# Optimization experiments

Measured on AMD Instinct MI355X. Metric: run time of the kernel, lower is better.

Reference implementation:

```python
import jax, jax.numpy as jnp
import numpy as np

N = 1000   # node count forced by fc1_1 in_features=1680 (see shape derivation)
E = 8000   # edges, avg degree ~8
F_IN = 6   # node feature dim (first 3 = pos, zeroed in forward)


def setup_inputs() -> dict:
    key = jax.random.key(0)
    ks = jax.random.split(key, 24)
    f = lambda k, s, sc=1.0: jax.random.normal(k, s, dtype=jnp.float32) * sc
    inp = {
        "x": f(ks[0], (N, F_IN)),
        "edge_index": jax.random.randint(ks[1], (2, E), 0, N, dtype=jnp.int64),
        # GCNConv weights (xavier-ish scale)
        "W1": f(ks[2], (F_IN, 32), 0.4), "b1": jnp.zeros((32,), jnp.float32),
        "W2": f(ks[3], (32, 32), 0.18), "b2": jnp.zeros((32,), jnp.float32),
        # Conv2d kernels, OIHW
        "k1": f(ks[4], (3, 1, 3, 2), 0.3), "kb1": jnp.zeros((3,), jnp.float32),
        "k2": f(ks[5], (6, 3, 3, 2), 0.2), "kb2": jnp.zeros((6,), jnp.float32),
        "k3": f(ks[6], (3, 6, 3, 2), 0.2), "kb3": jnp.zeros((3,), jnp.float32),
        "k4": f(ks[7], (1, 3, 3, 2), 0.2), "kb4": jnp.zeros((1,), jnp.float32),
        # FC head (torch Linear layout: [out, in])
        "fw1": f(ks[8], (1024, 1680), 0.02), "fb1": jnp.zeros((1024,), jnp.float32),
        "fw2": f(ks[9], (1024, 1024), 0.03), "fb2": jnp.zeros((1024,), jnp.float32),
        "fw3": f(ks[10], (64, 1024), 0.03), "fb3": jnp.zeros((64,), jnp.float32),
    }
    return inp


def _conv2d(x, w, b):
    out = jax.lax.conv_general_dilated(
        x, w, window_strides=(1, 1), padding="VALID",
        dimension_numbers=("NCHW", "OIHW", "NCHW"))
    return out + b[None, :, None, None]


def _maxpool2(x):  # MaxPool2d((2,1), stride=(2,1))
    return jax.lax.reduce_window(x, -jnp.inf, jax.lax.max,
                                 (1, 1, 2, 1), (1, 1, 2, 1), "VALID")


def reference(x, edge_index, W1, b1, W2, b2, k1, kb1, k2, kb2, k3, kb3, k4, kb4,
              fw1, fb1, fw2, fb2, fw3, fb3):
    num_nodes = x.shape[0]
    # forward zeroes the first 3 features (positions)
    x = x.at[:, :3].set(0.0)

    loop = jnp.arange(num_nodes)
    row = jnp.concatenate([edge_index[0], loop])
    col = jnp.concatenate([edge_index[1], loop])
    deg = jnp.zeros((num_nodes,), x.dtype).at[col].add(1.0)
    dinv = jnp.where(deg > 0, jax.lax.rsqrt(deg), 0.0)
    norm = (dinv[row] * dinv[col])[:, None]  # [E+N, 1]

    def gcn(h, W, b):
        hw = h @ W                                   # [N, 32]
        msg = hw[row] * norm                         # gather + scale
        return jax.ops.segment_sum(msg, col, num_segments=num_nodes) + b

    leaky = lambda v: jnp.where(v > 0, v, 0.2 * v)   # LeakyReLU(0.2)
    h = leaky(gcn(x, W1, b1))
    h = leaky(gcn(h, W2, b2))                        # [N, 32]

    img = h[None, None]                              # [1, 1, N, 32]
    img = _maxpool2(jax.nn.relu(_conv2d(img, k1, kb1)))   # [1,3,499,31]
    img = _maxpool2(jax.nn.relu(_conv2d(img, k2, kb2)))   # [1,6,248,30]
    img = _maxpool2(jax.nn.relu(_conv2d(img, k3, kb3)))   # [1,3,123,29]
    img = _maxpool2(jax.nn.relu(_conv2d(img, k4, kb4)))   # [1,1,60,28]

    v = img.reshape(-1)                              # [1680]
    v = v @ fw1.T + fb1                              # no activation between FCs (as in source)
    v = v @ fw2.T + fb2
    v = v @ fw3.T + fb3                              # [64]
    return v
```

## Files before the change

kernel.cpp:

```cpp
#include <hip/hip_runtime.h>

#define LEAKY(v) ((v) > 0.0f ? (v) : 0.2f * (v))

__global__ void k1_prep(const float* __restrict__ x, const int* __restrict__ col,
                        const float* __restrict__ W1, float* __restrict__ deg,
                        float* __restrict__ aggs ,
                        float* __restrict__ xw, int n, int E) {
    int tid = blockIdx.x * blockDim.x + threadIdx.x;
    int NT = gridDim.x * blockDim.x;
    for (int i = tid; i < 2 * n * 32; i += NT) aggs[i] = 0.0f;
    for (int e = tid; e < E; e += NT) atomicAdd(&deg[col[e]], 1.0f);
    for (int t = tid; t < n * 32; t += NT) {
        int j = t & 31, nn = t >> 5;
        xw[t] = x[nn*6+3] * W1[96+j]
              + x[nn*6+4] * W1[128+j]
              + x[nn*6+5] * W1[160+j];
    }
}

__global__ void k_scatter(const float* __restrict__ xw, const float* __restrict__ deg,
                          const int* __restrict__ row, const int* __restrict__ col,
                          float* __restrict__ agg, int E, int n) {
    int tid = blockIdx.x * blockDim.x + threadIdx.x;
    int total = (E + n) * 32;
    if (tid >= total) return;
    int e = tid >> 5, j = tid & 31;
    int r, c; float nrm;
    if (e < E) {
        r = row[e]; c = col[e];
        nrm = (1.0f / sqrtf(deg[r] + 1.0f)) * (1.0f / sqrtf(deg[c] + 1.0f));
    } else {
        r = c = e - E;
        nrm = 1.0f / (deg[r] + 1.0f);
    }
    atomicAdd(&agg[c * 32 + j], xw[r * 32 + j] * nrm);
}

__global__ void k3_xw2(const float* __restrict__ agg1, const float* __restrict__ b1,
                       const float* __restrict__ W2, float* __restrict__ xw, int n) {
    int tid = blockIdx.x * blockDim.x + threadIdx.x;
    if (tid >= n * 32) return;
    int j = tid & 31, nn = tid >> 5;
    const float* a = agg1 + nn * 32;
    float s = 0.0f;
#pragma unroll
    for (int f = 0; f < 32; ++f) {
        float v = a[f] + b1[f];
        v = LEAKY(v);
        s += v * W2[f * 32 + j];
    }
    xw[tid] = s;
}

__global__ void k5_conv1(const float* __restrict__ h2, const float* __restrict__ b2,
                         const float* __restrict__ w, const float* __restrict__ bias,
                         float* __restrict__ out) {
    const int Hp = 499, Wo = 31, total = 3 * Hp * Wo;
    int t0 = blockIdx.x * blockDim.x + threadIdx.x;
    if (t0 >= total) return;
    int ow = t0 % Wo; int t = t0 / Wo; int oh = t % Hp; int co = t / Hp;
    const float* ip = h2 + (2 * oh) * 32 + ow;
    float vals[4][2];
#pragma unroll
    for (int r = 0; r < 4; ++r)
#pragma unroll
        for (int cx = 0; cx < 2; ++cx) {
            float v = ip[r * 32 + cx] + b2[ow + cx];
            vals[r][cx] = LEAKY(v);
        }
    const float* wp = w + co * 6;
    float a0 = vals[0][0]*wp[0] + vals[0][1]*wp[1] + vals[1][0]*wp[2]
             + vals[1][1]*wp[3] + vals[2][0]*wp[4] + vals[2][1]*wp[5];
    float a1 = vals[1][0]*wp[0] + vals[1][1]*wp[1] + vals[2][0]*wp[2]
             + vals[2][1]*wp[3] + vals[3][0]*wp[4] + vals[3][1]*wp[5];
    float m = fmaxf(a0, a1) + bias[co];
    out[t0] = fmaxf(m, 0.0f);
}

__global__ void k6_conv2(const float* __restrict__ in, const float* __restrict__ w,
                         const float* __restrict__ bias, float* __restrict__ out) {
    const int CI = 3, Hin = 499, Win = 31, Hp = 248, Wo = 30, total = 6 * Hp * Wo;
    int t0 = blockIdx.x * blockDim.x + threadIdx.x;
    if (t0 >= total) return;
    int ow = t0 % Wo; int t = t0 / Wo; int oh = t % Hp; int co = t / Hp;
    float a0 = 0.0f, a1 = 0.0f;
#pragma unroll
    for (int ci = 0; ci < CI; ++ci) {
        const float* q = in + (ci * Hin + 2 * oh) * Win + ow;
        const float* wp = w + (co * CI + ci) * 6;
        float r00 = q[0],     r01 = q[1];
        float r10 = q[Win],   r11 = q[Win+1];
        float r20 = q[2*Win], r21 = q[2*Win+1];
        float r30 = q[3*Win], r31 = q[3*Win+1];
        a0 += r00*wp[0] + r01*wp[1] + r10*wp[2] + r11*wp[3] + r20*wp[4] + r21*wp[5];
        a1 += r10*wp[0] + r11*wp[1] + r20*wp[2] + r21*wp[3] + r30*wp[4] + r31*wp[5];
    }
    float m = fmaxf(a0, a1) + bias[co];
    out[t0] = fmaxf(m, 0.0f);
}

__global__ void k7_conv3(const float* __restrict__ in, const float* __restrict__ w,
                         const float* __restrict__ bias, float* __restrict__ out) {
    const int CI = 6, Hin = 248, Win = 30, Hp = 123, Wo = 29, total = 3 * Hp * Wo;
    int t0 = blockIdx.x * blockDim.x + threadIdx.x;
    if (t0 >= total) return;
    int ow = t0 % Wo; int t = t0 / Wo; int oh = t % Hp; int co = t / Hp;
    float a0 = 0.0f, a1 = 0.0f;
#pragma unroll
    for (int ci = 0; ci < CI; ++ci) {
        const float* q = in + (ci * Hin + 2 * oh) * Win + ow;
        const float* wp = w + (co * CI + ci) * 6;
        float r00 = q[0],     r01 = q[1];
        float r10 = q[Win],   r11 = q[Win+1];
        float r20 = q[2*Win], r21 = q[2*Win+1];
        float r30 = q[3*Win], r31 = q[3*Win+1];
        a0 += r00*wp[0] + r01*wp[1] + r10*wp[2] + r11*wp[3] + r20*wp[4] + r21*wp[5];
        a1 += r10*wp[0] + r11*wp[1] + r20*wp[2] + r21*wp[3] + r30*wp[4] + r31*wp[5];
    }
    float m = fmaxf(a0, a1) + bias[co];
    out[t0] = fmaxf(m, 0.0f);
}

__global__ __launch_bounds__(256) void k8_conv4_fc1(
        const float* __restrict__ c3, const float* __restrict__ k4,
        const float* __restrict__ kb4, const float* __restrict__ fw1,
        const float* __restrict__ fb1, float* __restrict__ f1) {
    __shared__ __align__(16) float lc4[1680];
    const int Hin = 123, Win = 29, Wo = 28;
    float kb = kb4[0];
    for (int t0 = (int)threadIdx.x; t0 < 1680; t0 += 256) {
        int ow = t0 % Wo; int oh = t0 / Wo;
        float a0 = 0.0f, a1 = 0.0f;
#pragma unroll
        for (int ci = 0; ci < 3; ++ci) {
            const float* q = c3 + (ci * Hin + 2 * oh) * Win + ow;
            const float* wp = k4 + ci * 6;
            float r00 = q[0],     r01 = q[1];
            float r10 = q[Win],   r11 = q[Win+1];
            float r20 = q[2*Win], r21 = q[2*Win+1];
            float r30 = q[3*Win], r31 = q[3*Win+1];
            a0 += r00*wp[0] + r01*wp[1] + r10*wp[2] + r11*wp[3] + r20*wp[4] + r21*wp[5];
            a1 += r10*wp[0] + r11*wp[1] + r20*wp[2] + r21*wp[3] + r30*wp[4] + r31*wp[5];
        }
        float m = fmaxf(a0, a1) + kb;
        lc4[t0] = fmaxf(m, 0.0f);
    }
    __syncthreads();
    int wv = threadIdx.x >> 6, lane = threadIdx.x & 63;
    int o = blockIdx.x * 4 + wv;
    const float4* wr = (const float4*)(fw1 + (size_t)o * 1680);
    const float4* vv = (const float4*)lc4;
    float s = 0.0f;
    for (int i = lane; i < 420; i += 64) {
        float4 a = vv[i], ww = wr[i];
        s += a.x*ww.x + a.y*ww.y + a.z*ww.z + a.w*ww.w;
    }
#pragma unroll
    for (int off = 32; off > 0; off >>= 1) s += __shfl_down(s, off, 64);
    if (lane == 0) f1[o] = s + fb1[o];
}

__global__ __launch_bounds__(256) void k_fc1024(const float* __restrict__ v,
                                                const float* __restrict__ w,
                                                const float* __restrict__ b,
                                                float* __restrict__ out) {
    int wv = threadIdx.x >> 6, lane = threadIdx.x & 63;
    int o = blockIdx.x * 4 + wv;
    const float4* wr = (const float4*)(w + (size_t)o * 1024);
    const float4* vv = (const float4*)v;
    float s = 0.0f;
#pragma unroll
    for (int i = 0; i < 4; ++i) {
        float4 a = vv[lane + 64*i], ww = wr[lane + 64*i];
        s += a.x*ww.x + a.y*ww.y + a.z*ww.z + a.w*ww.w;
    }
#pragma unroll
    for (int off = 32; off > 0; off >>= 1) s += __shfl_down(s, off, 64);
    if (lane == 0) out[o] = s + b[o];
}

extern "C" void kernel_launch(void* const* d_in, const int* in_sizes, int n_in,
                              void* d_out, int out_size, void* d_ws, size_t ws_size,
                              hipStream_t stream) {
    const float* x   = (const float*)d_in[0];
    const int*   ei  = (const int*)d_in[1];
    const float* W1  = (const float*)d_in[2];
    const float* b1  = (const float*)d_in[3];
    const float* W2  = (const float*)d_in[4];
    const float* b2  = (const float*)d_in[5];
    const float* k1  = (const float*)d_in[6];
    const float* kb1 = (const float*)d_in[7];
    const float* k2  = (const float*)d_in[8];
    const float* kb2 = (const float*)d_in[9];
    const float* k3  = (const float*)d_in[10];
    const float* kb3 = (const float*)d_in[11];
    const float* k4  = (const float*)d_in[12];
    const float* kb4 = (const float*)d_in[13];
    const float* fw1 = (const float*)d_in[14];
    const float* fb1 = (const float*)d_in[15];
    const float* fw2 = (const float*)d_in[16];
    const float* fb2 = (const float*)d_in[17];
    const float* fw3 = (const float*)d_in[18];
    const float* fb3 = (const float*)d_in[19];

    int n = in_sizes[0] / 6;
    int E = in_sizes[1] / 2;
    const int* row = ei;
    const int* col = ei + E;

    float* ws   = (float*)d_ws;
    float* deg  = ws;
    float* agg1 = ws + 1024;
    float* agg2 = agg1 + 32000;
    float* xw   = agg2 + 32000;
    float* c1   = xw + 32000;
    float* c2   = c1 + 46407;
    float* c3   = c2 + 44640;
    float* f1   = c3 + 10704;
    float* f2   = f1 + 1024;

    const int B = 256;

    hipMemsetAsync(deg, 0, n * sizeof(float), stream);
    k1_prep<<<256, B, 0, stream>>>(x, col, W1, deg, agg1, xw, n, E);
    int st = (E + n) * 32;
    k_scatter<<<(st + B - 1) / B, B, 0, stream>>>(xw, deg, row, col, agg1, E, n);
    k3_xw2<<<(n * 32 + B - 1) / B, B, 0, stream>>>(agg1, b1, W2, xw, n);
    k_scatter<<<(st + B - 1) / B, B, 0, stream>>>(xw, deg, row, col, agg2, E, n);
    k5_conv1<<<(3 * 499 * 31 + B - 1) / B, B, 0, stream>>>(agg2, b2, k1, kb1, c1);
    k6_conv2<<<(6 * 248 * 30 + B - 1) / B, B, 0, stream>>>(c1, k2, kb2, c2);
    k7_conv3<<<(3 * 123 * 29 + B - 1) / B, B, 0, stream>>>(c2, k3, kb3, c3);
    k8_conv4_fc1<<<256, B, 0, stream>>>(c3, k4, kb4, fw1, fb1, f1);
    k_fc1024<<<256, B, 0, stream>>>(f1, fw2, fb2, f2);
    k_fc1024<<<16, B, 0, stream>>>(f2, fw3, fb3, (float*)d_out);
}
```

Measured before the change: 136.0 us.

## Fuse GCN, conv and FC stages and fold fw3·fw2 into a combined matrix

Cuts the pipeline from eleven launches to six. Degrees are now computed by per-node wave reductions over the column array, which removes the memset and the atomic degree pass. The X·W products are computed inside the scatter kernels, and conv1–conv3 are fused into one kernel that recomputes intermediates in registers. The second and third FC layers are folded into a 64x1024 matrix M = fw3·fw2, built each call inside the prep kernel, plus a bias term fw3·fb2. The trade-off is redundant recomputation in the fused conv and scatter kernels, and a 64M-FMA matrix product on only 64 blocks whose cost depends on overlapping with the other prep work.

```diff
diff --git a/kernel.cpp b/kernel.cpp
--- a/kernel.cpp
+++ b/kernel.cpp
@@ -2,25 +2,46 @@
 
 #define LEAKY(v) ((v) > 0.0f ? (v) : 0.2f * (v))
 
-__global__ void k1_prep(const float* __restrict__ x, const int* __restrict__ col,
-                        const float* __restrict__ W1, float* __restrict__ deg,
-                        float* __restrict__ aggs ,
-                        float* __restrict__ xw, int n, int E) {
-    int tid = blockIdx.x * blockDim.x + threadIdx.x;
-    int NT = gridDim.x * blockDim.x;
-    for (int i = tid; i < 2 * n * 32; i += NT) aggs[i] = 0.0f;
-    for (int e = tid; e < E; e += NT) atomicAdd(&deg[col[e]], 1.0f);
-    for (int t = tid; t < n * 32; t += NT) {
-        int j = t & 31, nn = t >> 5;
-        xw[t] = x[nn*6+3] * W1[96+j]
-              + x[nn*6+4] * W1[128+j]
-              + x[nn*6+5] * W1[160+j];
-    }
-}
-
-__global__ void k_scatter(const float* __restrict__ xw, const float* __restrict__ deg,
-                          const int* __restrict__ row, const int* __restrict__ col,
-                          float* __restrict__ agg, int E, int n) {
+__global__ __launch_bounds__(256) void kA_prep(
+        const int* __restrict__ col, const float* __restrict__ fw2,
+        const float* __restrict__ fw3, float* __restrict__ deg,
+        float* __restrict__ aggs ,
+        float* __restrict__ M, int n, int E) {
+    int T = blockIdx.x * 256 + (int)threadIdx.x;
+    if (T < 2 * n * 32) aggs[T] = 0.0f;
+    int wave = T >> 6, lane = T & 63;
+    if (wave < n) {
+        int cnt = 0;
+        for (int e = lane; e < E; e += 64) cnt += (col[e] == wave) ? 1 : 0;
+#pragma unroll
+        for (int off = 32; off > 0; off >>= 1) cnt += __shfl_down(cnt, off, 64);
+        if (lane == 0) deg[wave] = (float)cnt;
+    }
+    if (blockIdx.x < 64) {
+        int it = (blockIdx.x & 15) * 64;
+        int kt = (blockIdx.x >> 4) * 16;
+        int w  = (int)threadIdx.x >> 6;
+        int i  = it + ((int)threadIdx.x & 63);
+        int k0 = kt + w * 4;
+        float a0 = 0.f, a1 = 0.f, a2 = 0.f, a3 = 0.f;
+        const float* f30 = fw3 + (size_t)k0 * 1024;
+        for (int j = 0; j < 1024; ++j) {
+            float wv = fw2[j * 1024 + i];
+            a0 += f30[j]        * wv;
+            a1 += f30[1024 + j] * wv;
+            a2 += f30[2048 + j] * wv;
+            a3 += f30[3072 + j] * wv;
+        }
+        M[(size_t)(k0 + 0) * 1024 + i] = a0;
+        M[(size_t)(k0 + 1) * 1024 + i] = a1;
+        M[(size_t)(k0 + 2) * 1024 + i] = a2;
+        M[(size_t)(k0 + 3) * 1024 + i] = a3;
+    }
+}
+
+__global__ void kB_scatter1(const float* __restrict__ x, const float* __restrict__ W1,
+        const float* __restrict__ deg, const int* __restrict__ row,
+        const int* __restrict__ col, float* __restrict__ agg1, int E, int n) {
     int tid = blockIdx.x * blockDim.x + threadIdx.x;
     int total = (E + n) * 32;
     if (tid >= total) return;
@@ -33,15 +54,27 @@
         r = c = e - E;
         nrm = 1.0f / (deg[r] + 1.0f);
     }
-    atomicAdd(&agg[c * 32 + j], xw[r * 32 + j] * nrm);
-}
-
-__global__ void k3_xw2(const float* __restrict__ agg1, const float* __restrict__ b1,
-                       const float* __restrict__ W2, float* __restrict__ xw, int n) {
+    float val = x[r*6+3] * W1[96+j] + x[r*6+4] * W1[128+j] + x[r*6+5] * W1[160+j];
+    atomicAdd(&agg1[c * 32 + j], val * nrm);
+}
+
+__global__ void kC_scatter2(const float* __restrict__ agg1, const float* __restrict__ b1,
+        const float* __restrict__ W2, const float* __restrict__ deg,
+        const int* __restrict__ row, const int* __restrict__ col,
+        float* __restrict__ agg2, int E, int n) {
     int tid = blockIdx.x * blockDim.x + threadIdx.x;
-    if (tid >= n * 32) return;
-    int j = tid & 31, nn = tid >> 5;
-    const float* a = agg1 + nn * 32;
+    int total = (E + n) * 32;
+    if (tid >= total) return;
+    int e = tid >> 5, j = tid & 31;
+    int r, c; float nrm;
+    if (e < E) {
+        r = row[e]; c = col[e];
+        nrm = (1.0f / sqrtf(deg[r] + 1.0f)) * (1.0f / sqrtf(deg[c] + 1.0f));
+    } else {
+        r = c = e - E;
+        nrm = 1.0f / (deg[r] + 1.0f);
+    }
+    const float* a = agg1 + r * 32;
     float s = 0.0f;
 #pragma unroll
     for (int f = 0; f < 32; ++f) {
@@ -49,79 +82,81 @@
         v = LEAKY(v);
         s += v * W2[f * 32 + j];
     }
-    xw[tid] = s;
-}
-
-__global__ void k5_conv1(const float* __restrict__ h2, const float* __restrict__ b2,
-                         const float* __restrict__ w, const float* __restrict__ bias,
-                         float* __restrict__ out) {
-    const int Hp = 499, Wo = 31, total = 3 * Hp * Wo;
-    int t0 = blockIdx.x * blockDim.x + threadIdx.x;
+    atomicAdd(&agg2[c * 32 + j], s * nrm);
+}
+
+__global__ __launch_bounds__(256) void kD_c3(const float* __restrict__ agg2,
+        const float* __restrict__ b2,
+        const float* __restrict__ k1w, const float* __restrict__ kb1,
+        const float* __restrict__ k2w, const float* __restrict__ kb2,
+        const float* __restrict__ k3w, const float* __restrict__ kb3,
+        float* __restrict__ c3) {
+    const int total = 3 * 123 * 29;
+    int t0 = blockIdx.x * 256 + (int)threadIdx.x;
     if (t0 >= total) return;
-    int ow = t0 % Wo; int t = t0 / Wo; int oh = t % Hp; int co = t / Hp;
-    const float* ip = h2 + (2 * oh) * 32 + ow;
-    float vals[4][2];
-#pragma unroll
-    for (int r = 0; r < 4; ++r)
-#pragma unroll
-        for (int cx = 0; cx < 2; ++cx) {
-            float v = ip[r * 32 + cx] + b2[ow + cx];
-            vals[r][cx] = LEAKY(v);
-        }
-    const float* wp = w + co * 6;
-    float a0 = vals[0][0]*wp[0] + vals[0][1]*wp[1] + vals[1][0]*wp[2]
-             + vals[1][1]*wp[3] + vals[2][0]*wp[4] + vals[2][1]*wp[5];
-    float a1 = vals[1][0]*wp[0] + vals[1][1]*wp[1] + vals[2][0]*wp[2]
-             + vals[2][1]*wp[3] + vals[3][0]*wp[4] + vals[3][1]*wp[5];
-    float m = fmaxf(a0, a1) + bias[co];
-    out[t0] = fmaxf(m, 0.0f);
-}
-
-__global__ void k6_conv2(const float* __restrict__ in, const float* __restrict__ w,
-                         const float* __restrict__ bias, float* __restrict__ out) {
-    const int CI = 3, Hin = 499, Win = 31, Hp = 248, Wo = 30, total = 6 * Hp * Wo;
-    int t0 = blockIdx.x * blockDim.x + threadIdx.x;
-    if (t0 >= total) return;
-    int ow = t0 % Wo; int t = t0 / Wo; int oh = t % Hp; int co = t / Hp;
-    float a0 = 0.0f, a1 = 0.0f;
-#pragma unroll
-    for (int ci = 0; ci < CI; ++ci) {
-        const float* q = in + (ci * Hin + 2 * oh) * Win + ow;
-        const float* wp = w + (co * CI + ci) * 6;
-        float r00 = q[0],     r01 = q[1];
-        float r10 = q[Win],   r11 = q[Win+1];
-        float r20 = q[2*Win], r21 = q[2*Win+1];
-        float r30 = q[3*Win], r31 = q[3*Win+1];
-        a0 += r00*wp[0] + r01*wp[1] + r10*wp[2] + r11*wp[3] + r20*wp[4] + r21*wp[5];
-        a1 += r10*wp[0] + r11*wp[1] + r20*wp[2] + r21*wp[3] + r30*wp[4] + r31*wp[5];
-    }
-    float m = fmaxf(a0, a1) + bias[co];
-    out[t0] = fmaxf(m, 0.0f);
-}
-
-__global__ void k7_conv3(const float* __restrict__ in, const float* __restrict__ w,
-                         const float* __restrict__ bias, float* __restrict__ out) {
-    const int CI = 6, Hin = 248, Win = 30, Hp = 123, Wo = 29, total = 3 * Hp * Wo;
-    int t0 = blockIdx.x * blockDim.x + threadIdx.x;
-    if (t0 >= total) return;
-    int ow = t0 % Wo; int t = t0 / Wo; int oh = t % Hp; int co = t / Hp;
-    float a0 = 0.0f, a1 = 0.0f;
-#pragma unroll
-    for (int ci = 0; ci < CI; ++ci) {
-        const float* q = in + (ci * Hin + 2 * oh) * Win + ow;
-        const float* wp = w + (co * CI + ci) * 6;
-        float r00 = q[0],     r01 = q[1];
-        float r10 = q[Win],   r11 = q[Win+1];
-        float r20 = q[2*Win], r21 = q[2*Win+1];
-        float r30 = q[3*Win], r31 = q[3*Win+1];
-        a0 += r00*wp[0] + r01*wp[1] + r10*wp[2] + r11*wp[3] + r20*wp[4] + r21*wp[5];
-        a1 += r10*wp[0] + r11*wp[1] + r20*wp[2] + r21*wp[3] + r30*wp[4] + r31*wp[5];
-    }
-    float m = fmaxf(a0, a1) + bias[co];
-    out[t0] = fmaxf(m, 0.0f);
-}
-
-__global__ __launch_bounds__(256) void k8_conv4_fc1(
+    int ow = t0 % 29; int tt = t0 / 29; int oh = tt % 123; int co = tt / 123;
+
+    float c1v[3][10][3];
+#pragma unroll
+    for (int ci = 0; ci < 3; ++ci) {
+        const float* kw = k1w + ci * 6;
+        float kb = kb1[ci];
+#pragma unroll
+        for (int hh = 0; hh < 10; ++hh) {
+            int r0 = (4 * oh + hh) * 2;
+#pragma unroll
+            for (int cc = 0; cc < 3; ++cc) {
+                int c0 = ow + cc;
+                float v[4][2];
+#pragma unroll
+                for (int rr = 0; rr < 4; ++rr)
+#pragma unroll
+                    for (int dc = 0; dc < 2; ++dc) {
+                        float u = agg2[(r0 + rr) * 32 + c0 + dc] + b2[c0 + dc];
+                        v[rr][dc] = LEAKY(u);
+                    }
+                float a0 = v[0][0]*kw[0] + v[0][1]*kw[1] + v[1][0]*kw[2]
+                         + v[1][1]*kw[3] + v[2][0]*kw[4] + v[2][1]*kw[5];
+                float a1 = v[1][0]*kw[0] + v[1][1]*kw[1] + v[2][0]*kw[2]
+                         + v[2][1]*kw[3] + v[3][0]*kw[4] + v[3][1]*kw[5];
+                c1v[ci][hh][cc] = fmaxf(fmaxf(a0, a1) + kb, 0.0f);
+            }
+        }
+    }
+
+    float A0 = 0.0f, A1 = 0.0f;
+#pragma unroll
+    for (int co2 = 0; co2 < 6; ++co2) {
+        float c2v[4][2];
+        float kb = kb2[co2];
+#pragma unroll
+        for (int r = 0; r < 4; ++r) {
+#pragma unroll
+            for (int c = 0; c < 2; ++c) {
+                float p0 = 0.0f, p1 = 0.0f;
+#pragma unroll
+                for (int ci = 0; ci < 3; ++ci) {
+                    const float* kw = k2w + (co2 * 3 + ci) * 6;
+                    p0 += c1v[ci][2*r  ][c]*kw[0] + c1v[ci][2*r  ][c+1]*kw[1]
+                        + c1v[ci][2*r+1][c]*kw[2] + c1v[ci][2*r+1][c+1]*kw[3]
+                        + c1v[ci][2*r+2][c]*kw[4] + c1v[ci][2*r+2][c+1]*kw[5];
+                    p1 += c1v[ci][2*r+1][c]*kw[0] + c1v[ci][2*r+1][c+1]*kw[1]
+                        + c1v[ci][2*r+2][c]*kw[2] + c1v[ci][2*r+2][c+1]*kw[3]
+                        + c1v[ci][2*r+3][c]*kw[4] + c1v[ci][2*r+3][c+1]*kw[5];
+                }
+                c2v[r][c] = fmaxf(fmaxf(p0, p1) + kb, 0.0f);
+            }
+        }
+        const float* kw3 = k3w + (co * 6 + co2) * 6;
+        A0 += c2v[0][0]*kw3[0] + c2v[0][1]*kw3[1] + c2v[1][0]*kw3[2]
+            + c2v[1][1]*kw3[3] + c2v[2][0]*kw3[4] + c2v[2][1]*kw3[5];
+        A1 += c2v[1][0]*kw3[0] + c2v[1][1]*kw3[1] + c2v[2][0]*kw3[2]
+            + c2v[2][1]*kw3[3] + c2v[3][0]*kw3[4] + c2v[3][1]*kw3[5];
+    }
+    c3[t0] = fmaxf(fmaxf(A0, A1) + kb3[co], 0.0f);
+}
+
+__global__ __launch_bounds__(256) void kE_conv4_fc1(
         const float* __restrict__ c3, const float* __restrict__ k4,
         const float* __restrict__ kb4, const float* __restrict__ fw1,
         const float* __restrict__ fb1, float* __restrict__ f1) {
@@ -146,7 +181,7 @@
         lc4[t0] = fmaxf(m, 0.0f);
     }
     __syncthreads();
-    int wv = threadIdx.x >> 6, lane = threadIdx.x & 63;
+    int wv = (int)threadIdx.x >> 6, lane = (int)threadIdx.x & 63;
     int o = blockIdx.x * 4 + wv;
     const float4* wr = (const float4*)(fw1 + (size_t)o * 1680);
     const float4* vv = (const float4*)lc4;
@@ -160,23 +195,27 @@
     if (lane == 0) f1[o] = s + fb1[o];
 }
 
-__global__ __launch_bounds__(256) void k_fc1024(const float* __restrict__ v,
-                                                const float* __restrict__ w,
-                                                const float* __restrict__ b,
-                                                float* __restrict__ out) {
-    int wv = threadIdx.x >> 6, lane = threadIdx.x & 63;
-    int o = blockIdx.x * 4 + wv;
-    const float4* wr = (const float4*)(w + (size_t)o * 1024);
-    const float4* vv = (const float4*)v;
+__global__ __launch_bounds__(256) void kF_head(const float* __restrict__ f1,
+        const float* __restrict__ M, const float* __restrict__ fw3,
+        const float* __restrict__ fb2, const float* __restrict__ fb3,
+        float* __restrict__ out) {
+    int wv = (int)threadIdx.x >> 6, lane = (int)threadIdx.x & 63;
+    int k = blockIdx.x * 4 + wv;
+    const float4* Mr = (const float4*)(M + (size_t)k * 1024);
+    const float4* vv = (const float4*)f1;
+    const float4* f3 = (const float4*)(fw3 + (size_t)k * 1024);
+    const float4* bb = (const float4*)fb2;
     float s = 0.0f;
 #pragma unroll
-    for (int i = 0; i < 4; ++i) {
-        float4 a = vv[lane + 64*i], ww = wr[lane + 64*i];
+    for (int i2 = 0; i2 < 4; ++i2) {
+        float4 a = vv[lane + 64*i2], ww = Mr[lane + 64*i2];
         s += a.x*ww.x + a.y*ww.y + a.z*ww.z + a.w*ww.w;
+        float4 c = bb[lane + 64*i2], w3 = f3[lane + 64*i2];
+        s += c.x*w3.x + c.y*w3.y + c.z*w3.z + c.w*w3.w;
     }
 #pragma unroll
     for (int off = 32; off > 0; off >>= 1) s += __shfl_down(s, off, 64);
-    if (lane == 0) out[o] = s + b[o];
+    if (lane == 0) out[k] = s + fb3[k];
 }
 
 extern "C" void kernel_launch(void* const* d_in, const int* in_sizes, int n_in,
@@ -212,25 +251,17 @@
     float* deg  = ws;
     float* agg1 = ws + 1024;
     float* agg2 = agg1 + 32000;
-    float* xw   = agg2 + 32000;
-    float* c1   = xw + 32000;
-    float* c2   = c1 + 46407;
-    float* c3   = c2 + 44640;
+    float* M    = agg2 + 32000;
+    float* c3   = M + 65536;
     float* f1   = c3 + 10704;
-    float* f2   = f1 + 1024;
 
     const int B = 256;
-
-    hipMemsetAsync(deg, 0, n * sizeof(float), stream);
-    k1_prep<<<256, B, 0, stream>>>(x, col, W1, deg, agg1, xw, n, E);
     int st = (E + n) * 32;
-    k_scatter<<<(st + B - 1) / B, B, 0, stream>>>(xw, deg, row, col, agg1, E, n);
-    k3_xw2<<<(n * 32 + B - 1) / B, B, 0, stream>>>(agg1, b1, W2, xw, n);
-    k_scatter<<<(st + B - 1) / B, B, 0, stream>>>(xw, deg, row, col, agg2, E, n);
-    k5_conv1<<<(3 * 499 * 31 + B - 1) / B, B, 0, stream>>>(agg2, b2, k1, kb1, c1);
-    k6_conv2<<<(6 * 248 * 30 + B - 1) / B, B, 0, stream>>>(c1, k2, kb2, c2);
-    k7_conv3<<<(3 * 123 * 29 + B - 1) / B, B, 0, stream>>>(c2, k3, kb3, c3);
-    k8_conv4_fc1<<<256, B, 0, stream>>>(c3, k4, kb4, fw1, fb1, f1);
-    k_fc1024<<<256, B, 0, stream>>>(f1, fw2, fb2, f2);
-    k_fc1024<<<16, B, 0, stream>>>(f2, fw3, fb3, (float*)d_out);
-}
+
+    kA_prep<<<256, B, 0, stream>>>(col, fw2, fw3, deg, agg1, M, n, E);
+    kB_scatter1<<<(st + B - 1) / B, B, 0, stream>>>(x, W1, deg, row, col, agg1, E, n);
+    kC_scatter2<<<(st + B - 1) / B, B, 0, stream>>>(agg1, b1, W2, deg, row, col, agg2, E, n);
+    kD_c3<<<(3 * 123 * 29 + B - 1) / B, B, 0, stream>>>(agg2, b2, k1, kb1, k2, kb2, k3, kb3, c3);
+    kE_conv4_fc1<<<256, B, 0, stream>>>(c3, k4, kb4, fw1, fb1, f1);
+    kF_head<<<16, B, 0, stream>>>(f1, M, fw3, fb2, fb3, (float*)d_out);
+}
```

Result: slower. 204.5 us (+50.3%).
